# Kernel optimization log

Measured on AMD Instinct MI355X. Metric: run time of the kernel, lower is better.

The kernel has to match this reference:

```python
import jax, jax.numpy as jnp
import numpy as np

HEADS = 8
EPS = 1e-4

def pixel_norm(x):
    # faithful to source: mean over dim=1 (token axis for [B,T,C] tensors)
    return x / jnp.sqrt(jnp.mean(x * x, axis=1, keepdims=True) + EPS)

def setup_inputs() -> dict:
    key = jax.random.key(0)
    ks = jax.random.split(key, 6)
    B, T, C = 4, 2048, 512
    s = 1.0 / np.sqrt(C)
    return {
        "hidden_states": jax.random.normal(ks[0], (B, T, C), jnp.float32),
        "Wq": jax.random.normal(ks[1], (C, C), jnp.float32) * s,
        "Wk": jax.random.normal(ks[2], (C, C), jnp.float32) * s,
        "Wv": jax.random.normal(ks[3], (C, C), jnp.float32) * s,
        "Wo": jax.random.normal(ks[4], (C, C), jnp.float32) * s,
        "bo": jnp.zeros((C,), jnp.float32),
    }

def reference(hidden_states, Wq, Wk, Wv, Wo, bo):
    B, T, C = hidden_states.shape
    H = HEADS
    d = C // H
    scale = 1.0 / np.sqrt(d)  # attn.scale = head_dim**-0.5
    residual = hidden_states

    q = pixel_norm(hidden_states @ Wq)  # [B,T,C]
    k = pixel_norm(hidden_states @ Wk)
    v = pixel_norm(hidden_states @ Wv)

    # head_to_batch_dim: [B,T,C] -> [B,H,T,d]
    def split_heads(x):
        return x.reshape(B, T, H, d).transpose(0, 2, 1, 3)
    q, k, v = split_heads(q), split_heads(k), split_heads(v)

    scores = jnp.einsum("bhqd,bhkd->bhqk", q, k) * scale
    probs = jax.nn.softmax(scores, axis=-1)
    out = jnp.einsum("bhqk,bhkd->bhqd", probs, v)  # [B,H,T,d]

    # batch_to_head_dim: [B,H,T,d] -> [B,T,C]
    out = out.transpose(0, 2, 1, 3).reshape(B, T, C)
    out = out @ Wo + bo  # to_out[0]; to_out[1] is dropout (identity in eval)
    out = out + residual  # residual_connection
    return out  # rescale_output_factor = 1.0
```

## Files before the change

### kernel.cpp

```cpp
#include <hip/hip_runtime.h>

#define Tt 2048
#define Cc 512
#define Bb 4
#define BC (Bb * Cc)

typedef __attribute__((ext_vector_type(4))) float f32x4;
typedef __attribute__((ext_vector_type(8))) _Float16 f16x8;
typedef __attribute__((ext_vector_type(4))) _Float16 f16x4;
typedef __attribute__((ext_vector_type(2))) _Float16 f16x2;

__global__ __launch_bounds__(256) void wsetup(
    const float* __restrict__ Wq, const float* __restrict__ Wk,
    const float* __restrict__ Wv, const float* __restrict__ Wo,
    _Float16* __restrict__ Wt)
{
    const int z = blockIdx.y;
    const float* W = (z == 0) ? Wq : (z == 1) ? Wk : (z == 2) ? Wv : Wo;
    const int k0 = (blockIdx.x >> 3) * 64, n0 = (blockIdx.x & 7) * 64;
    const int tid = threadIdx.x;
    __shared__ float tile[64][65];

#pragma unroll
    for (int i = 0; i < 4; ++i) {
        const int idx = i * 256 + tid;
        const int kr = idx >> 4, c4 = idx & 15;
        float4 v = *(const float4*)&W[(size_t)(k0 + kr) * Cc + n0 + c4 * 4];
        tile[kr][c4 * 4 + 0] = v.x; tile[kr][c4 * 4 + 1] = v.y;
        tile[kr][c4 * 4 + 2] = v.z; tile[kr][c4 * 4 + 3] = v.w;
    }
    __syncthreads();
#pragma unroll
    for (int i = 0; i < 4; ++i) {
        const int idx = i * 256 + tid;
        const int nr = idx >> 4, k4 = idx & 15;
        f16x4 o;
        o[0] = (_Float16)tile[k4 * 4 + 0][nr];
        o[1] = (_Float16)tile[k4 * 4 + 1][nr];
        o[2] = (_Float16)tile[k4 * 4 + 2][nr];
        o[3] = (_Float16)tile[k4 * 4 + 3][nr];
        *(f16x4*)&Wt[((size_t)(z * 512 + n0 + nr)) * Cc + k0 + k4 * 4] = o;
    }
}

__global__ __launch_bounds__(256) void hs_half(
    const float* __restrict__ HS, _Float16* __restrict__ HSh)
{
    const size_t i = ((size_t)blockIdx.x * 256 + threadIdx.x) * 8;
    float4 a = *(const float4*)&HS[i];
    float4 b = *(const float4*)&HS[i + 4];
    f16x8 o;
    o[0] = (_Float16)a.x; o[1] = (_Float16)a.y;
    o[2] = (_Float16)a.z; o[3] = (_Float16)a.w;
    o[4] = (_Float16)b.x; o[5] = (_Float16)b.y;
    o[6] = (_Float16)b.z; o[7] = (_Float16)b.w;
    *(f16x8*)&HSh[i] = o;
}

__global__ __launch_bounds__(256, 3) void qkv_mfma(
    const _Float16* __restrict__ HSh, const _Float16* __restrict__ Wt,
    _Float16* __restrict__ Qf, _Float16* __restrict__ Kf,
    _Float16* __restrict__ Vf, float* __restrict__ colsum)
{
    const int mt = blockIdx.x;
    const int nt = blockIdx.y;
    const int z  = blockIdx.z;
    _Float16* Out = (z == 0) ? Qf : (z == 1) ? Kf : Vf;

    const int tid = threadIdx.x;
    const int wave = tid >> 6, lane = tid & 63;
    const int quad = lane >> 4, lm = lane & 15;
    const int wm = (wave & 1) * 64, wn = (wave >> 1) * 64;

    __shared__ _Float16 sA[128 * 40];
    __shared__ _Float16 sB[128 * 40];

    f32x4 acc[4][4];
#pragma unroll
    for (int mf = 0; mf < 4; ++mf)
#pragma unroll
        for (int nf = 0; nf < 4; ++nf) acc[mf][nf] = (f32x4){0.f, 0.f, 0.f, 0.f};

    const int r2 = tid >> 1, kc = (tid & 1) * 16;
    const _Float16* ga = HSh + (size_t)(mt * 128 + r2) * Cc + kc;
    const _Float16* gb = Wt + ((size_t)(z * 512 + nt * 128 + r2)) * Cc + kc;

    for (int k0 = 0; k0 < Cc; k0 += 32) {
        __syncthreads();
        {
            *(f16x8*)&sA[r2 * 40 + kc]     = *(const f16x8*)&ga[k0];
            *(f16x8*)&sA[r2 * 40 + kc + 8] = *(const f16x8*)&ga[k0 + 8];
            *(f16x8*)&sB[r2 * 40 + kc]     = *(const f16x8*)&gb[k0];
            *(f16x8*)&sB[r2 * 40 + kc + 8] = *(const f16x8*)&gb[k0 + 8];
        }
        __syncthreads();

        f16x8 ah[4], bh[4];
#pragma unroll
        for (int mf = 0; mf < 4; ++mf)
            ah[mf] = *(const f16x8*)&sA[(wm + mf * 16 + lm) * 40 + quad * 8];
#pragma unroll
        for (int nf = 0; nf < 4; ++nf)
            bh[nf] = *(const f16x8*)&sB[(wn + nf * 16 + lm) * 40 + quad * 8];
#pragma unroll
        for (int mf = 0; mf < 4; ++mf)
#pragma unroll
            for (int nf = 0; nf < 4; ++nf)
                acc[mf][nf] = __builtin_amdgcn_mfma_f32_16x16x32_f16(ah[mf], bh[nf], acc[mf][nf], 0, 0, 0);
    }

    const int bidx = mt >> 4;
#pragma unroll
    for (int nf = 0; nf < 4; ++nf) {
        float cs = 0.f;
#pragma unroll
        for (int mf = 0; mf < 4; ++mf)
#pragma unroll
            for (int r = 0; r < 4; ++r) {
                const float v = acc[mf][nf][r];
                const size_t idx =
                    (size_t)(mt * 128 + wm + mf * 16 + quad * 4 + r) * Cc +
                    nt * 128 + wn + nf * 16 + lm;
                Out[idx] = (_Float16)v;
                cs += v * v;
            }
        cs += __shfl_xor(cs, 16, 64);
        cs += __shfl_xor(cs, 32, 64);
        if (lane < 16)
            atomicAdd(&colsum[(size_t)z * BC + bidx * Cc + nt * 128 + wn + nf * 16 + lane], cs);
    }
}

__global__ void inv_norm_kernel(const float* __restrict__ colsum,
                                float* __restrict__ inv)
{
    const int i = blockIdx.x * blockDim.x + threadIdx.x;
    if (i < 3 * BC) inv[i] = rsqrtf(colsum[i] * (1.0f / Tt) + 1e-4f);
}

__global__ __launch_bounds__(256) void norm_vt(
    const _Float16* __restrict__ V, _Float16* __restrict__ VT)
{
    const int blk = blockIdx.x;
    const int b = blk >> 8, ct = (blk >> 5) & 7, tt = blk & 31;
    const int t0 = tt * 64, c0 = ct * 64;
    const int tid = threadIdx.x;

    __shared__ _Float16 tile[64 * 72];

#pragma unroll
    for (int i = 0; i < 2; ++i) {
        const int idx = i * 256 + tid;
        const int tr = idx >> 3, c8 = (idx & 7) * 8;
        *(f16x8*)&tile[tr * 72 + c8] =
            *(const f16x8*)&V[(size_t)(b * Tt + t0 + tr) * Cc + c0 + c8];
    }
    __syncthreads();
#pragma unroll
    for (int i = 0; i < 2; ++i) {
        const int idx = i * 256 + tid;
        const int cr = idx >> 3, u = idx & 7;
        const int C0 = ((u >> 2) & 1) * 32 + (u & 1) * 16 + ((u >> 1) & 1) * 4;
        f16x4 oa, ob;
#pragma unroll
        for (int j = 0; j < 4; ++j) oa[j] = tile[(u * 8 + j) * 72 + cr];
#pragma unroll
        for (int j = 0; j < 4; ++j) ob[j] = tile[(u * 8 + 4 + j) * 72 + cr];
        _Float16* dst = &VT[(size_t)(b * Cc + c0 + cr) * Tt + t0];
        *(f16x4*)&dst[C0]     = oa;
        *(f16x4*)&dst[C0 + 8] = ob;
    }
}

#define LSTR 72

__global__ __launch_bounds__(256, 3) void attn_mfma(
    const _Float16* __restrict__ Qf, const _Float16* __restrict__ Kf,
    const _Float16* __restrict__ VT, const float* __restrict__ inv,
    _Float16* __restrict__ AO)
{
    const int bid = blockIdx.x;
    const int qt = bid >> 5;
    const int bh = bid & 31;
    const int b = bh >> 3, h = bh & 7;
    const int tid = threadIdx.x;
    const int wave = tid >> 6, lane = tid & 63;
    const int quad = lane >> 4, lm = lane & 15;

    __shared__ _Float16 sK[2][64 * LSTR];
    __shared__ _Float16 sVT[2][64 * LSTR];

    f16x8 qb[2][2];
    {
        const float* iqp = inv + b * Cc + h * 64;
        const float* ikp = inv + BC + b * Cc + h * 64;
#pragma unroll
        for (int qf = 0; qf < 2; ++qf) {
            const int row = qt * 128 + wave * 32 + qf * 16 + lm;
#pragma unroll
            for (int ks = 0; ks < 2; ++ks) {
                const int d0 = ks * 32 + quad * 8;
                f16x8 qv = *(const f16x8*)&Qf[(size_t)(b * Tt + row) * Cc + h * 64 + d0];
#pragma unroll
                for (int j = 0; j < 8; ++j) {
                    const float f = (float)qv[j] * iqp[d0 + j] * ikp[d0 + j] * 0.18033688011f;
                    qb[qf][ks][j] = (_Float16)f;
                }
            }
        }
    }

    f32x4 o[4][2];
#pragma unroll
    for (int cf = 0; cf < 4; ++cf)
#pragma unroll
        for (int qf = 0; qf < 2; ++qf) o[cf][qf] = (f32x4){0.f, 0.f, 0.f, 0.f};
    f32x4 ol[2];
#pragma unroll
    for (int qf = 0; qf < 2; ++qf) ol[qf] = (f32x4){0.f, 0.f, 0.f, 0.f};
    f16x8 ones;
#pragma unroll
    for (int j = 0; j < 8; ++j) ones[j] = (_Float16)1.0f;

    f16x8 pb[2][2];
#pragma unroll
    for (int qf = 0; qf < 2; ++qf)
#pragma unroll
        for (int ks = 0; ks < 2; ++ks)
#pragma unroll
            for (int j = 0; j < 8; ++j) pb[qf][ks][j] = (_Float16)0.0f;

    const int sr0 = tid >> 3, sc0 = (tid & 7) * 8;
    const int sr1 = sr0 + 32;
    const _Float16* gK = Kf + (size_t)b * Tt * Cc + h * 64;
    const _Float16* gV = VT + ((size_t)b * Cc + h * 64) * Tt;

    f16x8 rk0, rk1, rv0, rv1;
    {
        rk0 = *(const f16x8*)&gK[(size_t)sr0 * Cc + sc0];
        rk1 = *(const f16x8*)&gK[(size_t)sr1 * Cc + sc0];
        rv0 = *(const f16x8*)&gV[(size_t)sr0 * Tt + sc0];
        rv1 = *(const f16x8*)&gV[(size_t)sr1 * Tt + sc0];
    }

    for (int kt = 0; kt < 32; ++kt) {
        const int cur = kt & 1, prv = cur ^ 1;
        _Float16* sKc = sK[cur];
        _Float16* sVc = sVT[cur];

        __syncthreads();
        *(f16x8*)&sKc[sr0 * LSTR + sc0] = rk0;
        *(f16x8*)&sKc[sr1 * LSTR + sc0] = rk1;
        *(f16x8*)&sVc[sr0 * LSTR + sc0] = rv0;
        *(f16x8*)&sVc[sr1 * LSTR + sc0] = rv1;
        __syncthreads();

        if (kt < 31) {
            const int t0 = (kt + 1) * 64;
            rk0 = *(const f16x8*)&gK[(size_t)(t0 + sr0) * Cc + sc0];
            rk1 = *(const f16x8*)&gK[(size_t)(t0 + sr1) * Cc + sc0];
            rv0 = *(const f16x8*)&gV[(size_t)sr0 * Tt + t0 + sc0];
            rv1 = *(const f16x8*)&gV[(size_t)sr1 * Tt + t0 + sc0];
        }

        f32x4 st[4][2];
#pragma unroll
        for (int kf = 0; kf < 4; ++kf)
#pragma unroll
            for (int qf = 0; qf < 2; ++qf) st[kf][qf] = (f32x4){0.f, 0.f, 0.f, 0.f};
#pragma unroll
        for (int ks = 0; ks < 2; ++ks) {
            f16x8 ka[4];
#pragma unroll
            for (int kf = 0; kf < 4; ++kf)
                ka[kf] = *(const f16x8*)&sKc[(kf * 16 + lm) * LSTR + ks * 32 + quad * 8];
#pragma unroll
            for (int kf = 0; kf < 4; ++kf)
#pragma unroll
                for (int qf = 0; qf < 2; ++qf)
                    st[kf][qf] = __builtin_amdgcn_mfma_f32_16x16x32_f16(ka[kf], qb[qf][ks], st[kf][qf], 0, 0, 0);
        }

        if (kt > 0) {
            _Float16* sVp = sVT[prv];
#pragma unroll
            for (int ks = 0; ks < 2; ++ks) {
                f16x8 va[4];
#pragma unroll
                for (int cf = 0; cf < 4; ++cf)
                    va[cf] = *(const f16x8*)&sVp[(cf * 16 + lm) * LSTR + ks * 32 + quad * 8];
#pragma unroll
                for (int cf = 0; cf < 4; ++cf)
#pragma unroll
                    for (int qf = 0; qf < 2; ++qf)
                        o[cf][qf] = __builtin_amdgcn_mfma_f32_16x16x32_f16(va[cf], pb[qf][ks], o[cf][qf], 0, 0, 0);
#pragma unroll
                for (int qf = 0; qf < 2; ++qf)
                    ol[qf] = __builtin_amdgcn_mfma_f32_16x16x32_f16(ones, pb[qf][ks], ol[qf], 0, 0, 0);
            }
        }

#pragma unroll
        for (int ks = 0; ks < 2; ++ks)
#pragma unroll
            for (int qf = 0; qf < 2; ++qf) {
                const f32x4 a = st[2 * ks][qf];
                const f32x4 c = st[2 * ks + 1][qf];
                const f16x2 l0 = __builtin_bit_cast(f16x2, __builtin_amdgcn_cvt_pkrtz(
                    __builtin_amdgcn_exp2f(a[0]), __builtin_amdgcn_exp2f(a[1])));
                const f16x2 l1 = __builtin_bit_cast(f16x2, __builtin_amdgcn_cvt_pkrtz(
                    __builtin_amdgcn_exp2f(a[2]), __builtin_amdgcn_exp2f(a[3])));
                const f16x2 h0 = __builtin_bit_cast(f16x2, __builtin_amdgcn_cvt_pkrtz(
                    __builtin_amdgcn_exp2f(c[0]), __builtin_amdgcn_exp2f(c[1])));
                const f16x2 h1 = __builtin_bit_cast(f16x2, __builtin_amdgcn_cvt_pkrtz(
                    __builtin_amdgcn_exp2f(c[2]), __builtin_amdgcn_exp2f(c[3])));
                f16x8 p;
                p[0] = l0[0]; p[1] = l0[1]; p[2] = l1[0]; p[3] = l1[1];
                p[4] = h0[0]; p[5] = h0[1]; p[6] = h1[0]; p[7] = h1[1];
                pb[qf][ks] = p;
            }
    }

    {
        _Float16* sVp = sVT[1];
#pragma unroll
        for (int ks = 0; ks < 2; ++ks) {
            f16x8 va[4];
#pragma unroll
            for (int cf = 0; cf < 4; ++cf)
                va[cf] = *(const f16x8*)&sVp[(cf * 16 + lm) * LSTR + ks * 32 + quad * 8];
#pragma unroll
            for (int cf = 0; cf < 4; ++cf)
#pragma unroll
                for (int qf = 0; qf < 2; ++qf)
                    o[cf][qf] = __builtin_amdgcn_mfma_f32_16x16x32_f16(va[cf], pb[qf][ks], o[cf][qf], 0, 0, 0);
#pragma unroll
            for (int qf = 0; qf < 2; ++qf)
                ol[qf] = __builtin_amdgcn_mfma_f32_16x16x32_f16(ones, pb[qf][ks], ol[qf], 0, 0, 0);
        }
    }

    float il[2];
#pragma unroll
    for (int qf = 0; qf < 2; ++qf) il[qf] = 1.0f / ol[qf][0];
    const float* ivp = inv + 2 * BC + b * Cc + h * 64;
    float iv[4][4];
#pragma unroll
    for (int cf = 0; cf < 4; ++cf) {
        float4 t = *(const float4*)&ivp[cf * 16 + quad * 4];
        iv[cf][0] = t.x; iv[cf][1] = t.y; iv[cf][2] = t.z; iv[cf][3] = t.w;
    }
#pragma unroll
    for (int qf = 0; qf < 2; ++qf) {
        const size_t row = (size_t)(b * Tt + qt * 128 + wave * 32 + qf * 16 + lm);
#pragma unroll
        for (int cf = 0; cf < 4; ++cf) {
            f16x4 pk;
#pragma unroll
            for (int r = 0; r < 4; ++r)
                pk[r] = (_Float16)(o[cf][qf][r] * il[qf] * iv[cf][r]);
            *(f16x4*)&AO[row * Cc + h * 64 + cf * 16 + quad * 4] = pk;
        }
    }
}

__global__ __launch_bounds__(256, 2) void out_mfma(
    const _Float16* __restrict__ AO, const _Float16* __restrict__ Wt,
    const float* __restrict__ bo, const float* __restrict__ HS,
    float* __restrict__ Outp)
{
    const int mt = blockIdx.x;
    const int nt = blockIdx.y;
    const int tid = threadIdx.x;
    const int wave = tid >> 6, lane = tid & 63;
    const int quad = lane >> 4, lm = lane & 15;
    const int wm = (wave & 1) * 32, wn = (wave >> 1) * 64;

    __shared__ _Float16 sA[64 * 40];
    __shared__ _Float16 sB[128 * 40];

    f32x4 acc[2][4];
#pragma unroll
    for (int mf = 0; mf < 2; ++mf)
#pragma unroll
        for (int nf = 0; nf < 4; ++nf) acc[mf][nf] = (f32x4){0.f, 0.f, 0.f, 0.f};

    const int ra = tid >> 2, ka = (tid & 3) * 8;
    const int rb = tid >> 1, kb = (tid & 1) * 16;
    const _Float16* gah = AO + (size_t)(mt * 64 + ra) * Cc + ka;
    const _Float16* gbh = Wt + ((size_t)(3 * 512 + nt * 128 + rb)) * Cc + kb;

    for (int k0 = 0; k0 < Cc; k0 += 32) {
        __syncthreads();
        {
            *(f16x8*)&sA[ra * 40 + ka] = *(const f16x8*)&gah[k0];
            *(f16x8*)&sB[rb * 40 + kb]     = *(const f16x8*)&gbh[k0];
            *(f16x8*)&sB[rb * 40 + kb + 8] = *(const f16x8*)&gbh[k0 + 8];
        }
        __syncthreads();

        f16x8 ah[2], bh[4];
#pragma unroll
        for (int mf = 0; mf < 2; ++mf)
            ah[mf] = *(const f16x8*)&sA[(wm + mf * 16 + lm) * 40 + quad * 8];
#pragma unroll
        for (int nf = 0; nf < 4; ++nf)
            bh[nf] = *(const f16x8*)&sB[(wn + nf * 16 + lm) * 40 + quad * 8];
#pragma unroll
        for (int mf = 0; mf < 2; ++mf)
#pragma unroll
            for (int nf = 0; nf < 4; ++nf)
                acc[mf][nf] = __builtin_amdgcn_mfma_f32_16x16x32_f16(ah[mf], bh[nf], acc[mf][nf], 0, 0, 0);
    }

#pragma unroll
    for (int mf = 0; mf < 2; ++mf)
#pragma unroll
        for (int r = 0; r < 4; ++r) {
            const size_t m = (size_t)(mt * 64 + wm + mf * 16 + quad * 4 + r);
#pragma unroll
            for (int nf = 0; nf < 4; ++nf) {
                const int col = nt * 128 + wn + nf * 16 + lm;
                Outp[m * Cc + col] = acc[mf][nf][r] + bo[col] + HS[m * Cc + col];
            }
        }
}

extern "C" void kernel_launch(void* const* d_in, const int* in_sizes, int n_in,
                              void* d_out, int out_size, void* d_ws,
                              size_t ws_size, hipStream_t stream)
{
    const float* HS = (const float*)d_in[0];
    const float* Wq = (const float*)d_in[1];
    const float* Wk = (const float*)d_in[2];
    const float* Wv = (const float*)d_in[3];
    const float* Wo = (const float*)d_in[4];
    const float* bo = (const float*)d_in[5];
    float* out = (float*)d_out;

    const size_t SZ = (size_t)Bb * Tt * Cc;
    _Float16* Qf  = (_Float16*)d_ws;
    _Float16* Kf  = Qf + SZ;
    _Float16* Vf  = Kf + SZ;
    _Float16* VTh = Vf + SZ;
    _Float16* AO  = VTh + SZ;
    _Float16* Wt  = AO + SZ;
    float* colsum = (float*)(Wt + 4 * Cc * Cc);
    float* inv    = colsum + 3 * BC;

    _Float16* HSh = VTh;

    (void)hipMemsetAsync(colsum, 0, 3 * BC * sizeof(float), stream);

    wsetup<<<dim3(64, 4), 256, 0, stream>>>(Wq, Wk, Wv, Wo, Wt);

    hs_half<<<2048, 256, 0, stream>>>(HS, HSh);

    qkv_mfma<<<dim3(64, 4, 3), 256, 0, stream>>>(HSh, Wt, Qf, Kf, Vf, colsum);

    inv_norm_kernel<<<(3 * BC + 255) / 256, 256, 0, stream>>>(colsum, inv);

    norm_vt<<<1024, 256, 0, stream>>>(Vf, VTh);

    attn_mfma<<<dim3(512), 256, 0, stream>>>(Qf, Kf, VTh, inv, AO);

    out_mfma<<<dim3(128, 4), 256, 0, stream>>>(AO, Wt, bo, HS, out);
}
```

Measured before the change: 167.0 us.

## Use direct global-to-LDS loads in GEMMs and raise MFMA priority in attention

Replaces the register-staged global-to-shared copies in the QKV and output-projection GEMMs with global_load_lds 16-byte direct loads, using an unpadded 32-element LDS row stride to match the per-wave contiguous write layout. This is meant to remove VGPR staging and the separate ds_write instructions. The attention loop gets unroll 2 and s_setprio around its MFMA blocks to favour matrix issue over other waves. Dropping the padding may add LDS bank conflicts on the fragment reads, and the direct loads are still bracketed by barriers, so there is no extra overlap.

```diff
diff --git a/kernel.cpp b/kernel.cpp
--- a/kernel.cpp
+++ b/kernel.cpp
@@ -9,6 +9,13 @@
 typedef __attribute__((ext_vector_type(8))) _Float16 f16x8;
 typedef __attribute__((ext_vector_type(4))) _Float16 f16x4;
 typedef __attribute__((ext_vector_type(2))) _Float16 f16x2;
+
+__device__ static inline void gl16(const _Float16* g, _Float16* l)
+{
+    __builtin_amdgcn_global_load_lds(
+        (const __attribute__((address_space(1))) void*)g,
+        (__attribute__((address_space(3))) void*)l, 16, 0, 0);
+}
 
 __global__ __launch_bounds__(256) void wsetup(
     const float* __restrict__ Wq, const float* __restrict__ Wk,
@@ -72,8 +79,8 @@
     const int quad = lane >> 4, lm = lane & 15;
     const int wm = (wave & 1) * 64, wn = (wave >> 1) * 64;
 
-    __shared__ _Float16 sA[128 * 40];
-    __shared__ _Float16 sB[128 * 40];
+    __shared__ _Float16 sA[128 * 32];
+    __shared__ _Float16 sB[128 * 32];
 
     f32x4 acc[4][4];
 #pragma unroll
@@ -81,27 +88,28 @@
 #pragma unroll
         for (int nf = 0; nf < 4; ++nf) acc[mf][nf] = (f32x4){0.f, 0.f, 0.f, 0.f};
 
-    const int r2 = tid >> 1, kc = (tid & 1) * 16;
-    const _Float16* ga = HSh + (size_t)(mt * 128 + r2) * Cc + kc;
-    const _Float16* gb = Wt + ((size_t)(z * 512 + nt * 128 + r2)) * Cc + kc;
+    const int lr = lane >> 2;
+    const int lc = (lane & 3) * 8;
+    const _Float16* gaA = HSh + (size_t)(mt * 128 + wave * 32 + lr) * Cc + lc;
+    const _Float16* gaB = Wt + ((size_t)(z * 512 + nt * 128 + wave * 32 + lr)) * Cc + lc;
+    _Float16* ldA = &sA[wave * 1024];
+    _Float16* ldB = &sB[wave * 1024];
 
     for (int k0 = 0; k0 < Cc; k0 += 32) {
         __syncthreads();
-        {
-            *(f16x8*)&sA[r2 * 40 + kc]     = *(const f16x8*)&ga[k0];
-            *(f16x8*)&sA[r2 * 40 + kc + 8] = *(const f16x8*)&ga[k0 + 8];
-            *(f16x8*)&sB[r2 * 40 + kc]     = *(const f16x8*)&gb[k0];
-            *(f16x8*)&sB[r2 * 40 + kc + 8] = *(const f16x8*)&gb[k0 + 8];
-        }
+        gl16(gaA + k0,            ldA);
+        gl16(gaA + 16 * Cc + k0,  ldA + 512);
+        gl16(gaB + k0,            ldB);
+        gl16(gaB + 16 * Cc + k0,  ldB + 512);
         __syncthreads();
 
         f16x8 ah[4], bh[4];
 #pragma unroll
         for (int mf = 0; mf < 4; ++mf)
-            ah[mf] = *(const f16x8*)&sA[(wm + mf * 16 + lm) * 40 + quad * 8];
+            ah[mf] = *(const f16x8*)&sA[(wm + mf * 16 + lm) * 32 + quad * 8];
 #pragma unroll
         for (int nf = 0; nf < 4; ++nf)
-            bh[nf] = *(const f16x8*)&sB[(wn + nf * 16 + lm) * 40 + quad * 8];
+            bh[nf] = *(const f16x8*)&sB[(wn + nf * 16 + lm) * 32 + quad * 8];
 #pragma unroll
         for (int mf = 0; mf < 4; ++mf)
 #pragma unroll
@@ -243,6 +251,7 @@
         rv1 = *(const f16x8*)&gV[(size_t)sr1 * Tt + sc0];
     }
 
+#pragma unroll 2
     for (int kt = 0; kt < 32; ++kt) {
         const int cur = kt & 1, prv = cur ^ 1;
         _Float16* sKc = sK[cur];
@@ -274,11 +283,13 @@
 #pragma unroll
             for (int kf = 0; kf < 4; ++kf)
                 ka[kf] = *(const f16x8*)&sKc[(kf * 16 + lm) * LSTR + ks * 32 + quad * 8];
+            __builtin_amdgcn_s_setprio(1);
 #pragma unroll
             for (int kf = 0; kf < 4; ++kf)
 #pragma unroll
                 for (int qf = 0; qf < 2; ++qf)
                     st[kf][qf] = __builtin_amdgcn_mfma_f32_16x16x32_f16(ka[kf], qb[qf][ks], st[kf][qf], 0, 0, 0);
+            __builtin_amdgcn_s_setprio(0);
         }
 
         if (kt > 0) {
@@ -289,6 +300,7 @@
 #pragma unroll
                 for (int cf = 0; cf < 4; ++cf)
                     va[cf] = *(const f16x8*)&sVp[(cf * 16 + lm) * LSTR + ks * 32 + quad * 8];
+                __builtin_amdgcn_s_setprio(1);
 #pragma unroll
                 for (int cf = 0; cf < 4; ++cf)
 #pragma unroll
@@ -297,6 +309,7 @@
 #pragma unroll
                 for (int qf = 0; qf < 2; ++qf)
                     ol[qf] = __builtin_amdgcn_mfma_f32_16x16x32_f16(ones, pb[qf][ks], ol[qf], 0, 0, 0);
+                __builtin_amdgcn_s_setprio(0);
             }
         }
 
@@ -376,8 +389,8 @@
     const int quad = lane >> 4, lm = lane & 15;
     const int wm = (wave & 1) * 32, wn = (wave >> 1) * 64;
 
-    __shared__ _Float16 sA[64 * 40];
-    __shared__ _Float16 sB[128 * 40];
+    __shared__ _Float16 sA[64 * 32];
+    __shared__ _Float16 sB[128 * 32];
 
     f32x4 acc[2][4];
 #pragma unroll
@@ -385,27 +398,27 @@
 #pragma unroll
         for (int nf = 0; nf < 4; ++nf) acc[mf][nf] = (f32x4){0.f, 0.f, 0.f, 0.f};
 
-    const int ra = tid >> 2, ka = (tid & 3) * 8;
-    const int rb = tid >> 1, kb = (tid & 1) * 16;
-    const _Float16* gah = AO + (size_t)(mt * 64 + ra) * Cc + ka;
-    const _Float16* gbh = Wt + ((size_t)(3 * 512 + nt * 128 + rb)) * Cc + kb;
+    const int lr = lane >> 2;
+    const int lc = (lane & 3) * 8;
+    const _Float16* gaA = AO + (size_t)(mt * 64 + wave * 16 + lr) * Cc + lc;
+    const _Float16* gaB = Wt + ((size_t)(3 * 512 + nt * 128 + wave * 32 + lr)) * Cc + lc;
+    _Float16* ldA = &sA[wave * 512];
+    _Float16* ldB = &sB[wave * 1024];
 
     for (int k0 = 0; k0 < Cc; k0 += 32) {
         __syncthreads();
-        {
-            *(f16x8*)&sA[ra * 40 + ka] = *(const f16x8*)&gah[k0];
-            *(f16x8*)&sB[rb * 40 + kb]     = *(const f16x8*)&gbh[k0];
-            *(f16x8*)&sB[rb * 40 + kb + 8] = *(const f16x8*)&gbh[k0 + 8];
-        }
+        gl16(gaA + k0,           ldA);
+        gl16(gaB + k0,           ldB);
+        gl16(gaB + 16 * Cc + k0, ldB + 512);
         __syncthreads();
 
         f16x8 ah[2], bh[4];
 #pragma unroll
         for (int mf = 0; mf < 2; ++mf)
-            ah[mf] = *(const f16x8*)&sA[(wm + mf * 16 + lm) * 40 + quad * 8];
+            ah[mf] = *(const f16x8*)&sA[(wm + mf * 16 + lm) * 32 + quad * 8];
 #pragma unroll
         for (int nf = 0; nf < 4; ++nf)
-            bh[nf] = *(const f16x8*)&sB[(wn + nf * 16 + lm) * 40 + quad * 8];
+            bh[nf] = *(const f16x8*)&sB[(wn + nf * 16 + lm) * 32 + quad * 8];
 #pragma unroll
         for (int mf = 0; mf < 2; ++mf)
 #pragma unroll
```

Result: faster. 163.0 us (-2.4%).
